# Kernel optimization log

Measured on AMD Instinct MI355X. Metric: run time of the kernel, lower is better.

Reference implementation:

```python
import jax, jax.numpy as jnp
import numpy as np

IN_DIM, HID_DIM, OUT_DIM = 256, 1024, 256
B, T = 256, 512

def setup_inputs() -> dict:
    key = jax.random.key(0)
    ks = jax.random.split(key, 7)
    s_x = 1.0 / np.sqrt(IN_DIM)
    s_h = 1.0 / np.sqrt(HID_DIM)
    return {
        "x": jax.random.normal(ks[0], (B, T, IN_DIM), dtype=jnp.float32),
        "Wx": jax.random.uniform(ks[1], (3 * HID_DIM, IN_DIM), jnp.float32, -s_x, s_x),
        "bx": jax.random.uniform(ks[2], (3 * HID_DIM,), jnp.float32, -s_x, s_x),
        "Wh": jax.random.uniform(ks[3], (3 * HID_DIM, HID_DIM), jnp.float32, -s_h, s_h),
        "bh": jax.random.uniform(ks[4], (3 * HID_DIM,), jnp.float32, -s_h, s_h),
        "Wf": jax.random.uniform(ks[5], (OUT_DIM, HID_DIM), jnp.float32, -s_h, s_h),
        "bf": jax.random.uniform(ks[6], (OUT_DIM,), jnp.float32, -s_h, s_h),
    }

def _gru(x, Wx, bx, Wh, bh):
    # Precompute input projections for all timesteps: [B,T,3H]
    x_proj = jnp.einsum('bti,gi->btg', x, Wx) + bx
    h0 = jnp.zeros((x.shape[0], Wh.shape[1]), dtype=x.dtype)

    def step(h_prev, xp_t):
        h_t = h_prev @ Wh.T + bh  # [B,3H]
        x_r, x_z, x_n = jnp.split(xp_t, 3, axis=1)
        h_r, h_z, h_n = jnp.split(h_t, 3, axis=1)
        r = jax.nn.sigmoid(x_r + h_r)
        z = jax.nn.sigmoid(x_z + h_z)
        n = jnp.tanh(x_n + r * h_n)
        h = (1.0 - z) * h_prev + z * n  # note: nonstandard (follows source)
        return h, None

    h_final, _ = jax.lax.scan(step, h0, jnp.swapaxes(x_proj, 0, 1))
    return h_final

def reference(x, Wx, bx, Wh, bh, Wf, bf):
    h = _gru(x, Wx, bx, Wh, bh)
    return h @ Wf.T + bf  # [B, out_dim]
```

## Files before the change

### kernel.cpp

```cpp
#include <hip/hip_runtime.h>
#include <math.h>
#include <stddef.h>

#define BB 256
#define TT 512
#define IND 256
#define HH 1024
#define KV 1280
#define NCH 40
#define XCH 8

typedef __attribute__((ext_vector_type(8))) short short8;
typedef __attribute__((ext_vector_type(4))) float f32x4;
#define MFMA __builtin_amdgcn_mfma_f32_16x16x32_bf16

typedef __attribute__((address_space(1))) const unsigned char gconst_b;
typedef __attribute__((address_space(3))) unsigned char lds_b;

__device__ __forceinline__ unsigned short bf16_rne(float f) {
  unsigned u = __builtin_bit_cast(unsigned, f);
  u += 0x7FFFu + ((u >> 16) & 1u);
  return (unsigned short)(u >> 16);
}
__device__ __forceinline__ float bf16_f(unsigned short h) {
  unsigned u = ((unsigned)h) << 16;
  return __builtin_bit_cast(float, u);
}
__device__ __forceinline__ void split3(float v, unsigned short& hi,
                                       unsigned short& mi, unsigned short& lo) {
  hi = bf16_rne(v);
  float r = v - bf16_f(hi);
  mi = bf16_rne(r);
  float r2 = r - bf16_f(mi);
  lo = bf16_rne(r2);
}

__global__ __launch_bounds__(256) void split_wcat(
    const float* __restrict__ Wx, const float* __restrict__ Wh,
    unsigned short* __restrict__ Wc)
{
  const int col = blockIdx.y;
  const int kv  = blockIdx.x * 256 + threadIdx.x;
  const float v = (kv < IND) ? Wx[(size_t)col * IND + kv]
                             : Wh[(size_t)col * HH + (kv - IND)];
  unsigned short a, b, c;
  split3(v, a, b, c);
  const size_t o = (size_t)col * KV + kv;
  const size_t ps = (size_t)3072 * KV;
  Wc[o] = a; Wc[o + ps] = b; Wc[o + 2 * ps] = c;
}

__global__ __launch_bounds__(256) void init_h(
    float* __restrict__ hf, unsigned short* __restrict__ ht)
{
  const int i = blockIdx.x * 256 + threadIdx.x;
  hf[i] = 0.f;
  ht[i] = 0; ht[i + BB * HH] = 0; ht[i + 2 * BB * HH] = 0;
}

__global__ __launch_bounds__(256, 1) void gru_step(
    const float* __restrict__ x,
    const unsigned short* __restrict__ Wc,
    const float* __restrict__ bx, const float* __restrict__ bh,
    const float* __restrict__ hf,
    const unsigned short* __restrict__ ht,
    float* __restrict__ hnf,
    unsigned short* __restrict__ hnt,
    int t)
{
  __shared__ unsigned short Bs[2 * 4608];

  const int id  = blockIdx.x;
  const int xcd = id & 7;
  const int sub = id >> 3;
  const int jt  = xcd * 8 + (sub & 7);
  const int mt  = sub >> 3;

  const int tid  = threadIdx.x;
  const int lane = tid & 63;
  const int wv   = tid >> 6;
  const int l15  = lane & 15;
  const int lko  = lane >> 4;
  const int r0   = mt * 64 + wv * 16;
  const int jj0  = jt * 16;

  const size_t wps = (size_t)3072 * KV;
  const size_t hps = (size_t)BB * HH;

  f32x4 aR0 = {0,0,0,0}, aR1 = {0,0,0,0};
  f32x4 aZ0 = {0,0,0,0}, aZ1 = {0,0,0,0};
  f32x4 aNx0 = {0,0,0,0}, aNx1 = {0,0,0,0};
  f32x4 aNh0 = {0,0,0,0}, aNh1 = {0,0,0,0};

#define STAGE(KC, BUF)                                                         \
  if (wv < 3) {                                                                \
    const unsigned short* wp_ = Wc + (size_t)wv * wps;                         \
    _Pragma("unroll")                                                          \
    for (int g = 0; g < 3; ++g) {                                              \
      const unsigned short* src_ =                                             \
          wp_ + (size_t)(g * HH + jj0 + l15) * KV + (KC) * 32 + lko * 8;       \
      __builtin_amdgcn_global_load_lds(                                        \
          (const gconst_b*)src_,                                               \
          (lds_b*)&Bs[(BUF) * 4608 + (wv * 3 + g) * 512], 16, 0, 0);           \
    }                                                                          \
  }

  short8 cah, cam, cal;
  short8 nah, nam, nal;

#define LOADA_H(KC, AH, AM, AL)                                                \
  {                                                                            \
    const unsigned short* hb_ =                                                \
        ht + (size_t)(r0 + l15) * HH + ((KC) - XCH) * 32 + lko * 8;            \
    AH = *reinterpret_cast<const short8*>(hb_);                                \
    AM = *reinterpret_cast<const short8*>(hb_ + hps);                          \
    AL = *reinterpret_cast<const short8*>(hb_ + 2 * hps);                      \
  }

#define LOADA_X(KC, AH, AM, AL)                                                \
  {                                                                            \
    const float* xb_ = x + ((size_t)(r0 + l15) * TT + t) * IND + (KC) * 32     \
                         + lko * 8;                                            \
    float xv_[8];                                                              \
    *reinterpret_cast<float4*>(&xv_[0]) =                                      \
        *reinterpret_cast<const float4*>(xb_);                                 \
    *reinterpret_cast<float4*>(&xv_[4]) =                                      \
        *reinterpret_cast<const float4*>(xb_ + 4);                             \
    _Pragma("unroll")                                                          \
    for (int e_ = 0; e_ < 8; ++e_) {                                           \
      unsigned short h_, m_, l_;                                               \
      split3(xv_[e_], h_, m_, l_);                                             \
      AH[e_] = (short)h_; AM[e_] = (short)m_; AL[e_] = (short)l_;              \
    }                                                                          \
  }

  STAGE(0, 0)
  LOADA_X(0, cah, cam, cal)

  for (int kc = 0; kc < NCH; ++kc) {
    __syncthreads();
    const int nk = kc + 1;
    if (nk < NCH) {
      STAGE(nk, nk & 1)
      if (nk < XCH) { LOADA_X(nk, nah, nam, nal) }
      else          { LOADA_H(nk, nah, nam, nal) }
    }

    const int bb = (kc & 1) * 4608;
    const int fo = lko * 128 + l15 * 8;
    #pragma unroll
    for (int g = 0; g < 3; ++g) {
      const short8 bh_ = *reinterpret_cast<const short8*>(&Bs[bb + g * 512 + fo]);
      const short8 bm_ = *reinterpret_cast<const short8*>(&Bs[bb + (3 + g) * 512 + fo]);
      const short8 bl_ = *reinterpret_cast<const short8*>(&Bs[bb + (6 + g) * 512 + fo]);
      f32x4 *p0, *p1;
      if (g == 0)      { p0 = &aR0;  p1 = &aR1; }
      else if (g == 1) { p0 = &aZ0;  p1 = &aZ1; }
      else if (kc < XCH) { p0 = &aNx0; p1 = &aNx1; }
      else             { p0 = &aNh0; p1 = &aNh1; }
      *p0 = MFMA(cah, bh_, *p0, 0, 0, 0);
      *p1 = MFMA(cah, bm_, *p1, 0, 0, 0);
      *p0 = MFMA(cam, bh_, *p0, 0, 0, 0);
      *p1 = MFMA(cah, bl_, *p1, 0, 0, 0);
      *p0 = MFMA(cam, bm_, *p0, 0, 0, 0);
      *p1 = MFMA(cal, bh_, *p1, 0, 0, 0);
    }
    cah = nah; cam = nam; cal = nal;
  }

  const int jj = jj0 + l15;
  const float bxr = bx[jj],          bhr = bh[jj];
  const float bxz = bx[HH + jj],     bhz = bh[HH + jj];
  const float bxn = bx[2 * HH + jj], bhn = bh[2 * HH + jj];
  #pragma unroll
  for (int i = 0; i < 4; ++i) {
    const int row = r0 + lko * 4 + i;
    const float sr = aR0[i] + aR1[i] + bxr + bhr;
    const float sz = aZ0[i] + aZ1[i] + bxz + bhz;
    const float xn = aNx0[i] + aNx1[i] + bxn;
    const float hn = aNh0[i] + aNh1[i] + bhn;
    const float r  = 1.f / (1.f + __expf(-sr));
    const float z  = 1.f / (1.f + __expf(-sz));
    const float n  = tanhf(xn + r * hn);
    const float hp = hf[(size_t)row * HH + jj];
    const float hv = (1.f - z) * hp + z * n;
    hnf[(size_t)row * HH + jj] = hv;
    unsigned short th, tm, tl;
    split3(hv, th, tm, tl);
    hnt[(size_t)row * HH + jj] = th;
    hnt[hps + (size_t)row * HH + jj] = tm;
    hnt[2 * hps + (size_t)row * HH + jj] = tl;
  }
#undef STAGE
#undef LOADA_H
#undef LOADA_X
}

__global__ __launch_bounds__(256) void final_gemm(
    const float* __restrict__ h, const float* __restrict__ Wf,
    const float* __restrict__ bf, float* __restrict__ out)
{
  __shared__ float As[32][36];
  __shared__ float Ws[32][36];
  const int tid = threadIdx.x;
  const int b0 = blockIdx.x * 32, o0 = blockIdx.y * 32;
  const int to = tid & 31, tb = tid >> 5;
  float acc[4] = {};
  for (int kc = 0; kc < HH; kc += 32) {
    __syncthreads();
    #pragma unroll
    for (int p = 0; p < 4; ++p) {
      const int f = tid + 256 * p;
      const int row = f >> 5, c = f & 31;
      As[c][row] = h[(size_t)(b0 + row) * HH + kc + c];
      Ws[c][row] = Wf[(size_t)(o0 + row) * HH + kc + c];
    }
    __syncthreads();
    #pragma unroll
    for (int c = 0; c < 32; ++c) {
      const float4 a = *reinterpret_cast<const float4*>(&As[c][tb * 4]);
      const float w = Ws[c][to];
      acc[0] += a.x * w; acc[1] += a.y * w; acc[2] += a.z * w; acc[3] += a.w * w;
    }
  }
  #pragma unroll
  for (int i = 0; i < 4; ++i)
    out[(size_t)(b0 + tb * 4 + i) * 256 + o0 + to] = acc[i] + bf[o0 + to];
}

extern "C" void kernel_launch(void* const* d_in, const int* in_sizes, int n_in,
                              void* d_out, int out_size, void* d_ws, size_t ws_size,
                              hipStream_t stream)
{
  const float* x  = (const float*)d_in[0];
  const float* Wx = (const float*)d_in[1];
  const float* bx = (const float*)d_in[2];
  const float* Wh = (const float*)d_in[3];
  const float* bh = (const float*)d_in[4];
  const float* Wf = (const float*)d_in[5];
  const float* bf = (const float*)d_in[6];
  float* out = (float*)d_out;

  float* wsf = (float*)d_ws;
  float* hf0 = wsf;
  float* hf1 = wsf + (size_t)BB * HH;
  unsigned short* Wc  = (unsigned short*)(wsf + 2 * (size_t)BB * HH);
  unsigned short* ht0 = Wc + (size_t)3 * 3072 * KV;
  unsigned short* ht1 = ht0 + (size_t)3 * BB * HH;

  split_wcat<<<dim3(5, 3072), 256, 0, stream>>>(Wx, Wh, Wc);
  init_h<<<dim3(1024), 256, 0, stream>>>(hf0, ht0);

  float* cf = hf0; float* nf = hf1;
  unsigned short* ct = ht0; unsigned short* nt_ = ht1;
  for (int t = 0; t < TT; ++t) {
    gru_step<<<dim3(256), 256, 0, stream>>>(x, Wc, bx, bh, cf, ct, nf, nt_, t);
    float* tf = cf; cf = nf; nf = tf;
    unsigned short* tt = ct; ct = nt_; nt_ = tt;
  }
  final_gemm<<<dim3(8, 8), 256, 0, stream>>>(cf, Wf, bf, out);
}
```

Baseline: 26.31 ms.

## Replace per-timestep launches with persistent cooperative kernel and grid barrier

Fuses the 512 per-timestep GRU kernel launches into one cooperative persistent kernel that loops over time. Blocks synchronise through an atomic-counter grid barrier with release fences, and hidden-state reads use agent-scope relaxed atomic loads so they bypass stale cache lines. This removes launch overhead and the inter-kernel gaps between steps. In exchange it adds spin-wait barrier cost, and it relies on all 256 blocks being co-resident and on the fences being correct.

```diff
diff --git a/kernel.cpp b/kernel.cpp
--- a/kernel.cpp
+++ b/kernel.cpp
@@ -16,6 +16,8 @@
 
 typedef __attribute__((address_space(1))) const unsigned char gconst_b;
 typedef __attribute__((address_space(3))) unsigned char lds_b;
+
+union U16 { unsigned long long u[2]; short8 s; };
 
 __device__ __forceinline__ unsigned short bf16_rne(float f) {
   unsigned u = __builtin_bit_cast(unsigned, f);
@@ -51,22 +53,22 @@
 }
 
 __global__ __launch_bounds__(256) void init_h(
-    float* __restrict__ hf, unsigned short* __restrict__ ht)
+    float* __restrict__ hf, unsigned short* __restrict__ ht,
+    unsigned* __restrict__ cnt)
 {
   const int i = blockIdx.x * 256 + threadIdx.x;
   hf[i] = 0.f;
   ht[i] = 0; ht[i + BB * HH] = 0; ht[i + 2 * BB * HH] = 0;
-}
-
-__global__ __launch_bounds__(256, 1) void gru_step(
+  if (i == 0) *cnt = 0u;
+}
+
+__global__ __launch_bounds__(256, 1) void gru_persist(
     const float* __restrict__ x,
     const unsigned short* __restrict__ Wc,
     const float* __restrict__ bx, const float* __restrict__ bh,
-    const float* __restrict__ hf,
-    const unsigned short* __restrict__ ht,
-    float* __restrict__ hnf,
-    unsigned short* __restrict__ hnt,
-    int t)
+    float* __restrict__ hf0, float* __restrict__ hf1,
+    unsigned short* __restrict__ ht0, unsigned short* __restrict__ ht1,
+    unsigned* __restrict__ cnt)
 {
   __shared__ unsigned short Bs[2 * 4608];
 
@@ -87,10 +89,10 @@
   const size_t wps = (size_t)3072 * KV;
   const size_t hps = (size_t)BB * HH;
 
-  f32x4 aR0 = {0,0,0,0}, aR1 = {0,0,0,0};
-  f32x4 aZ0 = {0,0,0,0}, aZ1 = {0,0,0,0};
-  f32x4 aNx0 = {0,0,0,0}, aNx1 = {0,0,0,0};
-  f32x4 aNh0 = {0,0,0,0}, aNh1 = {0,0,0,0};
+  const int jj = jj0 + l15;
+  const float bxr = bx[jj],          bhr = bh[jj];
+  const float bxz = bx[HH + jj],     bhz = bh[HH + jj];
+  const float bxn = bx[2 * HH + jj], bhn = bh[2 * HH + jj];
 
 #define STAGE(KC, BUF)                                                         \
   if (wv < 3) {                                                                \
@@ -105,16 +107,21 @@
     }                                                                          \
   }
 
-  short8 cah, cam, cal;
-  short8 nah, nam, nal;
-
 #define LOADA_H(KC, AH, AM, AL)                                                \
   {                                                                            \
     const unsigned short* hb_ =                                                \
-        ht + (size_t)(r0 + l15) * HH + ((KC) - XCH) * 32 + lko * 8;            \
-    AH = *reinterpret_cast<const short8*>(hb_);                                \
-    AM = *reinterpret_cast<const short8*>(hb_ + hps);                          \
-    AL = *reinterpret_cast<const short8*>(hb_ + 2 * hps);                      \
+        htc + (size_t)(r0 + l15) * HH + ((KC) - XCH) * 32 + lko * 8;           \
+    const unsigned long long* q0_ = (const unsigned long long*)hb_;            \
+    const unsigned long long* q1_ = (const unsigned long long*)(hb_ + hps);    \
+    const unsigned long long* q2_ = (const unsigned long long*)(hb_ + 2*hps);  \
+    U16 t0_, t1_, t2_;                                                         \
+    t0_.u[0] = __hip_atomic_load(q0_,   __ATOMIC_RELAXED, __HIP_MEMORY_SCOPE_AGENT); \
+    t0_.u[1] = __hip_atomic_load(q0_+1, __ATOMIC_RELAXED, __HIP_MEMORY_SCOPE_AGENT); \
+    t1_.u[0] = __hip_atomic_load(q1_,   __ATOMIC_RELAXED, __HIP_MEMORY_SCOPE_AGENT); \
+    t1_.u[1] = __hip_atomic_load(q1_+1, __ATOMIC_RELAXED, __HIP_MEMORY_SCOPE_AGENT); \
+    t2_.u[0] = __hip_atomic_load(q2_,   __ATOMIC_RELAXED, __HIP_MEMORY_SCOPE_AGENT); \
+    t2_.u[1] = __hip_atomic_load(q2_+1, __ATOMIC_RELAXED, __HIP_MEMORY_SCOPE_AGENT); \
+    AH = t0_.s; AM = t1_.s; AL = t2_.s;                                        \
   }
 
 #define LOADA_X(KC, AH, AM, AL)                                                \
@@ -134,62 +141,87 @@
     }                                                                          \
   }
 
-  STAGE(0, 0)
-  LOADA_X(0, cah, cam, cal)
-
-  for (int kc = 0; kc < NCH; ++kc) {
-    __syncthreads();
-    const int nk = kc + 1;
-    if (nk < NCH) {
-      STAGE(nk, nk & 1)
-      if (nk < XCH) { LOADA_X(nk, nah, nam, nal) }
-      else          { LOADA_H(nk, nah, nam, nal) }
-    }
-
-    const int bb = (kc & 1) * 4608;
-    const int fo = lko * 128 + l15 * 8;
+  for (int t = 0; t < TT; ++t) {
+    const float* hfc          = (t & 1) ? hf1 : hf0;
+    float* hfn                = (t & 1) ? hf0 : hf1;
+    const unsigned short* htc = (t & 1) ? ht1 : ht0;
+    unsigned short* htn       = (t & 1) ? ht0 : ht1;
+
+    f32x4 aR0 = {0,0,0,0}, aR1 = {0,0,0,0};
+    f32x4 aZ0 = {0,0,0,0}, aZ1 = {0,0,0,0};
+    f32x4 aNx0 = {0,0,0,0}, aNx1 = {0,0,0,0};
+    f32x4 aNh0 = {0,0,0,0}, aNh1 = {0,0,0,0};
+
+    short8 cah, cam, cal, nah, nam, nal;
+
+    STAGE(0, 0)
+    LOADA_X(0, cah, cam, cal)
+
+    for (int kc = 0; kc < NCH; ++kc) {
+      __syncthreads();
+      const int nk = kc + 1;
+      if (nk < NCH) {
+        STAGE(nk, nk & 1)
+        if (nk < XCH) { LOADA_X(nk, nah, nam, nal) }
+        else          { LOADA_H(nk, nah, nam, nal) }
+      }
+
+      const int bb = (kc & 1) * 4608;
+      const int fo = lko * 128 + l15 * 8;
+      #pragma unroll
+      for (int g = 0; g < 3; ++g) {
+        const short8 bh_ = *reinterpret_cast<const short8*>(&Bs[bb + g * 512 + fo]);
+        const short8 bm_ = *reinterpret_cast<const short8*>(&Bs[bb + (3 + g) * 512 + fo]);
+        const short8 bl_ = *reinterpret_cast<const short8*>(&Bs[bb + (6 + g) * 512 + fo]);
+        f32x4 *p0, *p1;
+        if (g == 0)        { p0 = &aR0;  p1 = &aR1; }
+        else if (g == 1)   { p0 = &aZ0;  p1 = &aZ1; }
+        else if (kc < XCH) { p0 = &aNx0; p1 = &aNx1; }
+        else               { p0 = &aNh0; p1 = &aNh1; }
+        *p0 = MFMA(cah, bh_, *p0, 0, 0, 0);
+        *p1 = MFMA(cah, bm_, *p1, 0, 0, 0);
+        *p0 = MFMA(cam, bh_, *p0, 0, 0, 0);
+        *p1 = MFMA(cah, bl_, *p1, 0, 0, 0);
+        *p0 = MFMA(cam, bm_, *p0, 0, 0, 0);
+        *p1 = MFMA(cal, bh_, *p1, 0, 0, 0);
+      }
+      cah = nah; cam = nam; cal = nal;
+    }
+
     #pragma unroll
-    for (int g = 0; g < 3; ++g) {
-      const short8 bh_ = *reinterpret_cast<const short8*>(&Bs[bb + g * 512 + fo]);
-      const short8 bm_ = *reinterpret_cast<const short8*>(&Bs[bb + (3 + g) * 512 + fo]);
-      const short8 bl_ = *reinterpret_cast<const short8*>(&Bs[bb + (6 + g) * 512 + fo]);
-      f32x4 *p0, *p1;
-      if (g == 0)      { p0 = &aR0;  p1 = &aR1; }
-      else if (g == 1) { p0 = &aZ0;  p1 = &aZ1; }
-      else if (kc < XCH) { p0 = &aNx0; p1 = &aNx1; }
-      else             { p0 = &aNh0; p1 = &aNh1; }
-      *p0 = MFMA(cah, bh_, *p0, 0, 0, 0);
-      *p1 = MFMA(cah, bm_, *p1, 0, 0, 0);
-      *p0 = MFMA(cam, bh_, *p0, 0, 0, 0);
-      *p1 = MFMA(cah, bl_, *p1, 0, 0, 0);
-      *p0 = MFMA(cam, bm_, *p0, 0, 0, 0);
-      *p1 = MFMA(cal, bh_, *p1, 0, 0, 0);
-    }
-    cah = nah; cam = nam; cal = nal;
-  }
-
-  const int jj = jj0 + l15;
-  const float bxr = bx[jj],          bhr = bh[jj];
-  const float bxz = bx[HH + jj],     bhz = bh[HH + jj];
-  const float bxn = bx[2 * HH + jj], bhn = bh[2 * HH + jj];
-  #pragma unroll
-  for (int i = 0; i < 4; ++i) {
-    const int row = r0 + lko * 4 + i;
-    const float sr = aR0[i] + aR1[i] + bxr + bhr;
-    const float sz = aZ0[i] + aZ1[i] + bxz + bhz;
-    const float xn = aNx0[i] + aNx1[i] + bxn;
-    const float hn = aNh0[i] + aNh1[i] + bhn;
-    const float r  = 1.f / (1.f + __expf(-sr));
-    const float z  = 1.f / (1.f + __expf(-sz));
-    const float n  = tanhf(xn + r * hn);
-    const float hp = hf[(size_t)row * HH + jj];
-    const float hv = (1.f - z) * hp + z * n;
-    hnf[(size_t)row * HH + jj] = hv;
-    unsigned short th, tm, tl;
-    split3(hv, th, tm, tl);
-    hnt[(size_t)row * HH + jj] = th;
-    hnt[hps + (size_t)row * HH + jj] = tm;
-    hnt[2 * hps + (size_t)row * HH + jj] = tl;
+    for (int i = 0; i < 4; ++i) {
+      const int row = r0 + lko * 4 + i;
+      const float sr = aR0[i] + aR1[i] + bxr + bhr;
+      const float sz = aZ0[i] + aZ1[i] + bxz + bhz;
+      const float xn = aNx0[i] + aNx1[i] + bxn;
+      const float hn = aNh0[i] + aNh1[i] + bhn;
+      const float r  = 1.f / (1.f + __expf(-sr));
+      const float z  = 1.f / (1.f + __expf(-sz));
+      const float n  = tanhf(xn + r * hn);
+      const unsigned hu = __hip_atomic_load(
+          (const unsigned*)&hfc[(size_t)row * HH + jj],
+          __ATOMIC_RELAXED, __HIP_MEMORY_SCOPE_AGENT);
+      const float hp = __builtin_bit_cast(float, hu);
+      const float hv = (1.f - z) * hp + z * n;
+      hfn[(size_t)row * HH + jj] = hv;
+      unsigned short th, tm, tl;
+      split3(hv, th, tm, tl);
+      htn[(size_t)row * HH + jj] = th;
+      htn[hps + (size_t)row * HH + jj] = tm;
+      htn[2 * hps + (size_t)row * HH + jj] = tl;
+    }
+
+    __syncthreads();
+    if (tid == 0) {
+      __builtin_amdgcn_fence(__ATOMIC_RELEASE, "agent");
+      __hip_atomic_fetch_add(cnt, 1u, __ATOMIC_RELEASE,
+                             __HIP_MEMORY_SCOPE_AGENT);
+      const unsigned tgt = 256u * (unsigned)(t + 1);
+      while (__hip_atomic_load(cnt, __ATOMIC_RELAXED,
+                               __HIP_MEMORY_SCOPE_AGENT) < tgt)
+        __builtin_amdgcn_s_sleep(2);
+    }
+    __syncthreads();
   }
 #undef STAGE
 #undef LOADA_H
@@ -247,16 +279,16 @@
   unsigned short* Wc  = (unsigned short*)(wsf + 2 * (size_t)BB * HH);
   unsigned short* ht0 = Wc + (size_t)3 * 3072 * KV;
   unsigned short* ht1 = ht0 + (size_t)3 * BB * HH;
+  unsigned* cnt = (unsigned*)(ht1 + (size_t)3 * BB * HH);
 
   split_wcat<<<dim3(5, 3072), 256, 0, stream>>>(Wx, Wh, Wc);
-  init_h<<<dim3(1024), 256, 0, stream>>>(hf0, ht0);
-
-  float* cf = hf0; float* nf = hf1;
-  unsigned short* ct = ht0; unsigned short* nt_ = ht1;
-  for (int t = 0; t < TT; ++t) {
-    gru_step<<<dim3(256), 256, 0, stream>>>(x, Wc, bx, bh, cf, ct, nf, nt_, t);
-    float* tf = cf; cf = nf; nf = tf;
-    unsigned short* tt = ct; ct = nt_; nt_ = tt;
-  }
-  final_gemm<<<dim3(8, 8), 256, 0, stream>>>(cf, Wf, bf, out);
-}
+  init_h<<<dim3(1024), 256, 0, stream>>>(hf0, ht0, cnt);
+
+  void* kargs[] = {(void*)&x, (void*)&Wc, (void*)&bx, (void*)&bh,
+                   (void*)&hf0, (void*)&hf1, (void*)&ht0, (void*)&ht1,
+                   (void*)&cnt};
+  hipLaunchCooperativeKernel(gru_persist, dim3(256), dim3(256), kargs, 0u,
+                             stream);
+
+  final_gemm<<<dim3(8, 8), 256, 0, stream>>>(hf0, Wf, bf, out);
+}
```

Result: slower. 38.34 ms (+45.7%).
